# Kernel tuning notes

Hardware: AMD Instinct MI355X
Metric: run time of the kernel (lower is better)

The kernel has to match this reference:

```python
import jax, jax.numpy as jnp
import numpy as np

L = 3          # num_layers
D = 512        # hidden_dim
B, N = 8, 1024
EPS = 1e-5


def layernorm(x, gamma, beta):
    mu = jnp.mean(x, axis=-1, keepdims=True)
    var = jnp.var(x, axis=-1, keepdims=True)
    return (x - mu) * jax.lax.rsqrt(var + EPS) * gamma + beta


def setup_inputs() -> dict:
    key = jax.random.key(0)
    ks = jax.random.split(key, 12)
    s = 1.0 / np.sqrt(D)
    node_features = jax.random.normal(ks[0], (B, N, D), dtype=jnp.float32)
    adjacency_matrix = jax.random.randint(ks[1], (B, N, N), 0, 2, dtype=jnp.int32)
    return {
        "node_features": node_features,
        "adjacency_matrix": adjacency_matrix,
        # attn_linear: Linear(2D, 1) -> weight [2D], bias scalar, per layer
        "attn_w": jax.random.normal(ks[2], (L, 2 * D), dtype=jnp.float32) * (1.0 / np.sqrt(2 * D)),
        "attn_b": jax.random.normal(ks[3], (L,), dtype=jnp.float32) * 0.01,
        "W1": jax.random.normal(ks[4], (L, D, 4 * D), dtype=jnp.float32) * s,
        "b1": jnp.zeros((L, 4 * D), dtype=jnp.float32),
        "W2": jax.random.normal(ks[5], (L, 4 * D, D), dtype=jnp.float32) * (1.0 / np.sqrt(4 * D)),
        "b2": jnp.zeros((L, D), dtype=jnp.float32),
        "g1": jnp.ones((L, D), dtype=jnp.float32),
        "beta1": jnp.zeros((L, D), dtype=jnp.float32),
        "g2": jnp.ones((L, D), dtype=jnp.float32),
        "beta2": jnp.zeros((L, D), dtype=jnp.float32),
    }


def reference(node_features, adjacency_matrix, attn_w, attn_b, W1, b1, W2, b2, g1, beta1, g2, beta2):
    n = adjacency_matrix.shape[-1]
    # adjacency + self loops; mask of allowed edges
    mask = (adjacency_matrix.astype(jnp.float32) + jnp.eye(n, dtype=jnp.float32)) > 0  # [B,N,N]
    x = node_features
    d = x.shape[-1]
    for l in range(attn_w.shape[0]):
        # score_ij = a1.h_i + a2.h_j + b  (== Linear(concat(h_i,h_j)))
        si = x @ attn_w[l, :d]           # [B,N]
        sj = x @ attn_w[l, d:]           # [B,N]
        scores = si[:, :, None] + sj[:, None, :] + attn_b[l]   # [B,N,N]
        scores = jnp.where(scores >= 0, scores, 0.2 * scores)  # LeakyReLU(0.2)
        scores = jnp.where(mask, scores, -jnp.inf)
        attn = jax.nn.softmax(scores, axis=-1)                  # diag always unmasked
        agg = jnp.einsum('bij,bjd->bid', attn, x)
        h = layernorm(x + agg, g1[l], beta1[l])
        ff = jax.nn.gelu(h @ W1[l] + b1[l], approximate=False) @ W2[l] + b2[l]
        x = layernorm(h + ff, g2[l], beta2[l])
    return x
```

## Files before the change

### kernel.cpp

```cpp
#include <hip/hip_runtime.h>
#include <math.h>

#define NB 8
#define NN 1024
#define DD 512

typedef unsigned short u16;
typedef unsigned int u32;
typedef unsigned long long u64;
typedef __attribute__((ext_vector_type(8))) short bfrag;
typedef __attribute__((ext_vector_type(4))) float ffrag;

__device__ __forceinline__ u16 f2b(float f) {
    union { float f; u32 u; } v; v.f = f;
    u32 r = v.u + 0x7fffu + ((v.u >> 16) & 1u);
    return (u16)(r >> 16);
}
__device__ __forceinline__ float b2f(u16 b) {
    union { u32 u; float f; } v; v.u = ((u32)b) << 16;
    return v.f;
}

__device__ __forceinline__ float gelu_cheap(float v) {
    float s = v * 0.70710678118654752f;
    float a = fabsf(s);
    float t = 1.0f / (1.0f + 0.3275911f * a);
    float p = ((((1.061405429f * t - 1.453152027f) * t + 1.421413741f) * t
                - 0.284496736f) * t + 0.254829592f) * t;
    float erfa = 1.0f - p * __expf(-a * a);
    float erfs = copysignf(erfa, s);
    return 0.5f * v * (1.0f + erfs);
}

__device__ __forceinline__ void gload_lds16(const void* g, void* l) {
    __builtin_amdgcn_global_load_lds(
        (const __attribute__((address_space(1))) void*)g,
        (__attribute__((address_space(3))) void*)l, 16, 0, 0);
}

__global__ __launch_bounds__(256) void mask_pack(const int* __restrict__ adj,
                                                 u64* __restrict__ mb) {
    int idx = blockIdx.x * 256 + threadIdx.x;
    int w = idx & 15;
    int bi = idx >> 4;
    int i = bi & 1023;
    const int4* p = (const int4*)(adj + (size_t)bi * NN + w * 64);
    u64 m = 0;
#pragma unroll
    for (int q = 0; q < 16; ++q) {
        int4 v = p[q];
        if (v.x > 0) m |= 1ull << (q * 4 + 0);
        if (v.y > 0) m |= 1ull << (q * 4 + 1);
        if (v.z > 0) m |= 1ull << (q * 4 + 2);
        if (v.w > 0) m |= 1ull << (q * 4 + 3);
    }
    if (w == (i >> 6)) m |= 1ull << (i & 63);
    mb[idx] = m;
}

__global__ __launch_bounds__(256) void transpose_cvt(
    const float* __restrict__ in, u16* __restrict__ out,
    int R, int C, size_t inStr, size_t outStr)
{
    __shared__ float tile[32][33];
    int z = blockIdx.z;
    int r0 = blockIdx.y * 32, c0 = blockIdx.x * 32;
    int t = threadIdx.x;
    int tr = t >> 3, tc = (t & 7) * 4;
    float4 v = *(const float4*)(in + inStr * z + (size_t)(r0 + tr) * C + c0 + tc);
    tile[tr][tc + 0] = v.x; tile[tr][tc + 1] = v.y;
    tile[tr][tc + 2] = v.z; tile[tr][tc + 3] = v.w;
    __syncthreads();
    u32 w0 = (u32)f2b(tile[tc + 0][tr]) | ((u32)f2b(tile[tc + 1][tr]) << 16);
    u32 w1 = (u32)f2b(tile[tc + 2][tr]) | ((u32)f2b(tile[tc + 3][tr]) << 16);
    uint2 wv; wv.x = w0; wv.y = w1;
    *(uint2*)(out + outStr * z + (size_t)(c0 + tr) * R + r0 + tc) = wv;
}

__global__ __launch_bounds__(256) void score_proj_kernel(
    const float* __restrict__ x, const float* __restrict__ w,
    float* __restrict__ si, float* __restrict__ sj)
{
    int wave = threadIdx.x >> 6;
    int lane = threadIdx.x & 63;
    int row = blockIdx.x * 4 + wave;
    const float4* xr = (const float4*)(x + (size_t)row * DD) + lane * 2;
    const float4* w1 = (const float4*)(w) + lane * 2;
    const float4* w2 = (const float4*)(w + DD) + lane * 2;
    float a = 0.f, b2 = 0.f;
#pragma unroll
    for (int c = 0; c < 2; ++c) {
        float4 xv = xr[c], wa = w1[c], wb = w2[c];
        a  += xv.x * wa.x + xv.y * wa.y + xv.z * wa.z + xv.w * wa.w;
        b2 += xv.x * wb.x + xv.y * wb.y + xv.z * wb.z + xv.w * wb.w;
    }
#pragma unroll
    for (int off = 32; off > 0; off >>= 1) {
        a  += __shfl_xor(a, off);
        b2 += __shfl_xor(b2, off);
    }
    if (lane == 0) { si[row] = a; sj[row] = b2; }
}

__global__ __launch_bounds__(256) void softmax_p(
    const float* __restrict__ si, const float* __restrict__ sj,
    const float* __restrict__ attn_b, const u64* __restrict__ mb,
    u16* __restrict__ P)
{
    __shared__ u16 sb[8 * NN];
    int b  = blockIdx.x >> 7;
    int i0 = (blockIdx.x & 127) * 8;
    int tid = threadIdx.x;
    int r = tid >> 5, l32 = tid & 31;
    int i = i0 + r;
    float bb = attn_b[0];
    float siv = si[b * NN + i];
    const float* sjb = sj + b * NN;
    const u64* mbr = mb + ((size_t)b * NN + i) * 16;

    float sv[32];
    float mx = -INFINITY;
#pragma unroll
    for (int q = 0; q < 32; ++q) {
        int j = q * 32 + l32;
        u64 w = mbr[q >> 1];
        int bit = ((q & 1) << 5) + l32;
        float s = siv + sjb[j] + bb;
        s = (s >= 0.f) ? s : 0.2f * s;
        s = ((w >> bit) & 1ull) ? s : -INFINITY;
        sv[q] = s;
        mx = fmaxf(mx, s);
    }
#pragma unroll
    for (int off = 16; off > 0; off >>= 1) mx = fmaxf(mx, __shfl_xor(mx, off, 32));
    float sum = 0.f;
#pragma unroll
    for (int q = 0; q < 32; ++q) {
        float p = __expf(sv[q] - mx);
        sv[q] = p;
        sum += p;
    }
#pragma unroll
    for (int off = 16; off > 0; off >>= 1) sum += __shfl_xor(sum, off, 32);
    float inv = 1.f / sum;
#pragma unroll
    for (int q = 0; q < 32; ++q)
        sb[r * NN + q * 32 + l32] = f2b(sv[q] * inv);
    __syncthreads();
    const uint4* src = (const uint4*)sb;
    uint4* dst = (uint4*)(P + ((size_t)b * NN + i0) * NN);
#pragma unroll
    for (int t = 0; t < 4; ++t) dst[t * 256 + tid] = src[t * 256 + tid];
}

template <int EPI>
__global__ __launch_bounds__(256) void gemm64(
    const u16* __restrict__ A, const u16* __restrict__ Bm,
    const float* __restrict__ bias, const void* __restrict__ res,
    void* __restrict__ Cout, int K, int N, int lda, int ldb,
    size_t aStr, size_t bStr, size_t cStr, size_t resStr)
{
    __shared__ __align__(16) u16 lds[24576];
    int z = blockIdx.z;
    int m0 = blockIdx.y * 64, n0 = blockIdx.x * 128;
    int tid = threadIdx.x;
    int lane = tid & 63, wv = tid >> 6;

    const u16* ag[2]; const u16* bg[4];
    u32 la[2], lb[4];
#pragma unroll
    for (int i = 0; i < 2; ++i) {
        int q = i * 256 + tid;
        int row = q >> 3, c = q & 7;
        ag[i] = A + aStr * z + (size_t)(m0 + row) * lda + (c ^ (row & 7)) * 8;
        la[i] = i * 2048 + wv * 512;
    }
#pragma unroll
    for (int i = 0; i < 4; ++i) {
        int q = i * 256 + tid;
        int row = q >> 3, c = q & 7;
        bg[i] = Bm + bStr * z + (size_t)(n0 + row) * ldb + (c ^ (row & 7)) * 8;
        lb[i] = 8192 + i * 2048 + wv * 512;
    }

    int mw = (wv >> 1) * 32, nw = (wv & 1) * 64;
    int lr = lane & 15, lq = lane >> 4;
    int sw = lr & 7;

    ffrag acc[2][4];
#pragma unroll
    for (int i = 0; i < 2; ++i)
#pragma unroll
        for (int j = 0; j < 4; ++j) acc[i][j] = (ffrag){0.f, 0.f, 0.f, 0.f};

#pragma unroll
    for (int i = 0; i < 2; ++i) gload_lds16(ag[i], &lds[la[i]]);
#pragma unroll
    for (int i = 0; i < 4; ++i) gload_lds16(bg[i], &lds[lb[i]]);

    for (int k0 = 0; k0 < K; k0 += 64) {
        int cur = (k0 >> 6) & 1;
        if (k0 + 64 < K) {
#pragma unroll
            for (int i = 0; i < 2; ++i)
                gload_lds16(ag[i] + k0 + 64, &lds[((cur ^ 1) << 12) + la[i]]);
#pragma unroll
            for (int i = 0; i < 4; ++i)
                gload_lds16(bg[i] + k0 + 64, &lds[((cur ^ 1) << 13) + lb[i]]);
            asm volatile("s_waitcnt vmcnt(6)" ::: "memory");
        } else {
            asm volatile("s_waitcnt vmcnt(0)" ::: "memory");
        }
        asm volatile("s_barrier" ::: "memory");

        const u16* Ab = &lds[cur << 12];
        const u16* Bb = &lds[8192 + (cur << 13)];
#pragma unroll
        for (int h = 0; h < 2; ++h) {
            bfrag af[2], bf[4];
#pragma unroll
            for (int i = 0; i < 2; ++i)
                af[i] = *(const bfrag*)&Ab[(mw + i * 16 + lr) * 64 + ((h * 4 + lq) ^ sw) * 8];
#pragma unroll
            for (int j = 0; j < 4; ++j)
                bf[j] = *(const bfrag*)&Bb[(nw + j * 16 + lr) * 64 + ((h * 4 + lq) ^ sw) * 8];
#pragma unroll
            for (int i = 0; i < 2; ++i)
#pragma unroll
                for (int j = 0; j < 4; ++j)
                    acc[i][j] = __builtin_amdgcn_mfma_f32_16x16x32_bf16(af[i], bf[j], acc[i][j], 0, 0, 0);
        }
        asm volatile("s_waitcnt lgkmcnt(0)\ns_barrier" ::: "memory");
    }

    float* Cf = (float*)Cout + cStr * z;
    u16*   Cb = (u16*)Cout + cStr * z;
    const float* resf = (const float*)res;
    const u16*   resb = (const u16*)res;
#pragma unroll
    for (int i = 0; i < 2; ++i) {
        int row = m0 + mw + i * 16 + lq * 4;
#pragma unroll
        for (int j = 0; j < 4; ++j) {
            int col = n0 + nw + j * 16 + lr;
            float bv = (EPI != 0) ? bias[col] : 0.f;
#pragma unroll
            for (int r = 0; r < 4; ++r) {
                float v = acc[i][j][r] + bv;
                size_t off = (size_t)(row + r) * N + col;
                if (EPI == 1) {
                    Cb[off] = f2b(gelu_cheap(v));
                } else if (EPI == 0) {
                    Cf[off] = v + resf[resStr * z + off];
                } else {
                    Cf[off] = v + b2f(resb[off]);
                }
            }
        }
    }
}

template <bool BF>
__global__ __launch_bounds__(256) void ln_kernel(
    const float* __restrict__ in, const float* __restrict__ g,
    const float* __restrict__ be, void* __restrict__ out)
{
    int row = blockIdx.x;
    int tid = threadIdx.x;
    const float2* rp = (const float2*)(in + (size_t)row * DD);
    float2 v = rp[tid];
    float s  = v.x + v.y;
    float ss = v.x * v.x + v.y * v.y;
#pragma unroll
    for (int off = 32; off > 0; off >>= 1) {
        s  += __shfl_xor(s, off);
        ss += __shfl_xor(ss, off);
    }
    __shared__ float sh[8];
    int wave = tid >> 6, lane = tid & 63;
    if (lane == 0) { sh[wave] = s; sh[4 + wave] = ss; }
    __syncthreads();
    float S  = sh[0] + sh[1] + sh[2] + sh[3];
    float SS = sh[4] + sh[5] + sh[6] + sh[7];
    float mean = S * (1.f / DD);
    float var  = SS * (1.f / DD) - mean * mean;
    var = fmaxf(var, 0.f);
    float rs = rsqrtf(var + 1e-5f);
    float2 gv = ((const float2*)g)[tid];
    float2 bv = ((const float2*)be)[tid];
    float ox = (v.x - mean) * rs * gv.x + bv.x;
    float oy = (v.y - mean) * rs * gv.y + bv.y;
    if (BF) {
        u32 w = (u32)f2b(ox) | ((u32)f2b(oy) << 16);
        ((u32*)out)[(size_t)row * (DD / 2) + tid] = w;
    } else {
        float2 o; o.x = ox; o.y = oy;
        ((float2*)out)[(size_t)row * (DD / 2) + tid] = o;
    }
}

extern "C" void kernel_launch(void* const* d_in, const int* in_sizes, int n_in,
                              void* d_out, int out_size, void* d_ws, size_t ws_size,
                              hipStream_t stream) {
    const float* nf     = (const float*)d_in[0];
    const int*   adj    = (const int*)d_in[1];
    const float* attn_w = (const float*)d_in[2];
    const float* attn_b = (const float*)d_in[3];
    const float* W1     = (const float*)d_in[4];
    const float* b1     = (const float*)d_in[5];
    const float* W2     = (const float*)d_in[6];
    const float* b2     = (const float*)d_in[7];
    const float* g1     = (const float*)d_in[8];
    const float* be1    = (const float*)d_in[9];
    const float* g2     = (const float*)d_in[10];
    const float* be2    = (const float*)d_in[11];
    float* out = (float*)d_out;

    char* wsb = (char*)d_ws;
    float* x_cur = (float*)(wsb);
    u16*   h_bf  = (u16*)(wsb + 16777216);
    char*  scr   = wsb + 25165824;
    u16*   P     = (u16*)scr;
    float* hres  = (float*)(scr + 16777216);
    u16*   mid   = (u16*)scr;
    u16*   xT    = (u16*)(wsb + 58720256);
    u16*   W1t   = (u16*)(wsb + 67108864);
    u16*   W2t   = (u16*)(wsb + 73400320);
    u64*   mask  = (u64*)(wsb + 79691776);
    float* si    = (float*)(wsb + 80740352);
    float* sj    = (float*)(wsb + 80773120);

    mask_pack<<<512, 256, 0, stream>>>(adj, mask);
    transpose_cvt<<<dim3(64, 16, 3), 256, 0, stream>>>(W1, W1t, 512, 2048,
                                                       (size_t)512 * 2048, (size_t)512 * 2048);
    transpose_cvt<<<dim3(16, 64, 3), 256, 0, stream>>>(W2, W2t, 2048, 512,
                                                       (size_t)2048 * 512, (size_t)2048 * 512);

    for (int l = 0; l < 3; ++l) {
        const float* xin = (l == 0) ? nf : x_cur;
        score_proj_kernel<<<2048, 256, 0, stream>>>(xin, attn_w + (size_t)l * 1024, si, sj);
        transpose_cvt<<<dim3(16, 32, 8), 256, 0, stream>>>(xin, xT, 1024, 512,
                                                           (size_t)NN * DD, (size_t)NN * DD);
        softmax_p<<<1024, 256, 0, stream>>>(si, sj, attn_b + l, mask, P);
        gemm64<0><<<dim3(4, 16, 8), 256, 0, stream>>>(
            P, xT, nullptr, xin, hres, 1024, 512, 1024, 1024,
            (size_t)NN * NN, (size_t)DD * NN, (size_t)NN * DD, (size_t)NN * DD);
        ln_kernel<true><<<8192, 256, 0, stream>>>(hres, g1 + (size_t)l * 512, be1 + (size_t)l * 512, h_bf);
        gemm64<1><<<dim3(16, 128, 1), 256, 0, stream>>>(
            h_bf, W1t + (size_t)l * 1048576, b1 + (size_t)l * 2048, nullptr, mid,
            512, 2048, 512, 512, 0, 0, 0, 0);
        gemm64<2><<<dim3(4, 128, 1), 256, 0, stream>>>(
            mid, W2t + (size_t)l * 1048576, b2 + (size_t)l * 512, h_bf, x_cur,
            2048, 512, 2048, 2048, 0, 0, 0, 0);
        void* lnout = (l == 2) ? (void*)out : (void*)x_cur;
        ln_kernel<false><<<8192, 256, 0, stream>>>(x_cur, g2 + (size_t)l * 512, be2 + (size_t)l * 512, lnout);
    }
}
```

Measured before the change: 474.9 us.

## Triple-buffer GEMM loads, swizzle workgroups, stage GELU output, fuse score projection into LN

The GEMM moves from double to triple buffering in LDS, so two K tiles are in flight while the current one is computed. Workgroup IDs are remapped in strides of eight to spread neighbouring tiles across XCDs. The GELU epilogue now writes through LDS so global stores are coalesced 16-byte writes. The per-layer score projection kernel is folded into the preceding LayerNorm for layers 1 and 2, removing a launch and a re-read of x. The larger LDS footprint may reduce occupancy.

```diff
diff --git a/kernel.cpp b/kernel.cpp
--- a/kernel.cpp
+++ b/kernel.cpp
@@ -160,9 +160,15 @@
     void* __restrict__ Cout, int K, int N, int lda, int ldb,
     size_t aStr, size_t bStr, size_t cStr, size_t resStr)
 {
-    __shared__ __align__(16) u16 lds[24576];
-    int z = blockIdx.z;
-    int m0 = blockIdx.y * 64, n0 = blockIdx.x * 128;
+    __shared__ __align__(16) u16 lds[36864];
+    int gx = gridDim.x, gy = gridDim.y;
+    int wg = blockIdx.x + gx * (blockIdx.y + gy * blockIdx.z);
+    int nwg = gx * gy * gridDim.z;
+    wg = (wg & 7) * (nwg >> 3) + (wg >> 3);
+    int z = wg / (gx * gy);
+    int rem = wg - z * (gx * gy);
+    int by = rem / gx, bx = rem - by * gx;
+    int m0 = by * 64, n0 = bx * 128;
     int tid = threadIdx.x;
     int lane = tid & 63, wv = tid >> 6;
 
@@ -180,7 +186,7 @@
         int q = i * 256 + tid;
         int row = q >> 3, c = q & 7;
         bg[i] = Bm + bStr * z + (size_t)(n0 + row) * ldb + (c ^ (row & 7)) * 8;
-        lb[i] = 8192 + i * 2048 + wv * 512;
+        lb[i] = 4096 + i * 2048 + wv * 512;
     }
 
     int mw = (wv >> 1) * 32, nw = (wv & 1) * 64;
@@ -193,28 +199,35 @@
 #pragma unroll
         for (int j = 0; j < 4; ++j) acc[i][j] = (ffrag){0.f, 0.f, 0.f, 0.f};
 
+    int nt = K >> 6;
 #pragma unroll
     for (int i = 0; i < 2; ++i) gload_lds16(ag[i], &lds[la[i]]);
 #pragma unroll
     for (int i = 0; i < 4; ++i) gload_lds16(bg[i], &lds[lb[i]]);
-
-    for (int k0 = 0; k0 < K; k0 += 64) {
-        int cur = (k0 >> 6) & 1;
-        if (k0 + 64 < K) {
-#pragma unroll
-            for (int i = 0; i < 2; ++i)
-                gload_lds16(ag[i] + k0 + 64, &lds[((cur ^ 1) << 12) + la[i]]);
-#pragma unroll
-            for (int i = 0; i < 4; ++i)
-                gload_lds16(bg[i] + k0 + 64, &lds[((cur ^ 1) << 13) + lb[i]]);
+#pragma unroll
+    for (int i = 0; i < 2; ++i) gload_lds16(ag[i] + 64, &lds[12288 + la[i]]);
+#pragma unroll
+    for (int i = 0; i < 4; ++i) gload_lds16(bg[i] + 64, &lds[12288 + lb[i]]);
+
+    int cur = 0, stg = 2;
+    for (int t = 0; t < nt; ++t) {
+        if (t + 2 < nt) {
+            int bb = stg * 12288;
+            int ko = (t + 2) * 64;
+#pragma unroll
+            for (int i = 0; i < 2; ++i) gload_lds16(ag[i] + ko, &lds[bb + la[i]]);
+#pragma unroll
+            for (int i = 0; i < 4; ++i) gload_lds16(bg[i] + ko, &lds[bb + lb[i]]);
+            asm volatile("s_waitcnt vmcnt(12)" ::: "memory");
+        } else if (t + 2 == nt) {
             asm volatile("s_waitcnt vmcnt(6)" ::: "memory");
         } else {
             asm volatile("s_waitcnt vmcnt(0)" ::: "memory");
         }
         asm volatile("s_barrier" ::: "memory");
 
-        const u16* Ab = &lds[cur << 12];
-        const u16* Bb = &lds[8192 + (cur << 13)];
+        const u16* Ab = &lds[cur * 12288];
+        const u16* Bb = &lds[cur * 12288 + 4096];
 #pragma unroll
         for (int h = 0; h < 2; ++h) {
             bfrag af[2], bf[4];
@@ -231,39 +244,65 @@
                     acc[i][j] = __builtin_amdgcn_mfma_f32_16x16x32_bf16(af[i], bf[j], acc[i][j], 0, 0, 0);
         }
         asm volatile("s_waitcnt lgkmcnt(0)\ns_barrier" ::: "memory");
+        cur = (cur == 2) ? 0 : cur + 1;
+        stg = (stg == 2) ? 0 : stg + 1;
     }
 
     float* Cf = (float*)Cout + cStr * z;
     u16*   Cb = (u16*)Cout + cStr * z;
     const float* resf = (const float*)res;
     const u16*   resb = (const u16*)res;
-#pragma unroll
-    for (int i = 0; i < 2; ++i) {
-        int row = m0 + mw + i * 16 + lq * 4;
-#pragma unroll
-        for (int j = 0; j < 4; ++j) {
-            int col = n0 + nw + j * 16 + lr;
-            float bv = (EPI != 0) ? bias[col] : 0.f;
-#pragma unroll
-            for (int r = 0; r < 4; ++r) {
-                float v = acc[i][j][r] + bv;
-                size_t off = (size_t)(row + r) * N + col;
-                if (EPI == 1) {
-                    Cb[off] = f2b(gelu_cheap(v));
-                } else if (EPI == 0) {
-                    Cf[off] = v + resf[resStr * z + off];
-                } else {
-                    Cf[off] = v + b2f(resb[off]);
+    if (EPI == 1) {
+        u16* sb = lds;
+#pragma unroll
+        for (int i = 0; i < 2; ++i) {
+            int rr = mw + i * 16 + lq * 4;
+#pragma unroll
+            for (int j = 0; j < 4; ++j) {
+                int cc = nw + j * 16 + lr;
+                float bv = bias[n0 + cc];
+#pragma unroll
+                for (int r = 0; r < 4; ++r)
+                    sb[(rr + r) * 136 + cc] = f2b(gelu_cheap(acc[i][j][r] + bv));
+            }
+        }
+        __syncthreads();
+        u16* Crow = Cb + (size_t)m0 * N + n0;
+#pragma unroll
+        for (int t = 0; t < 4; ++t) {
+            int q = t * 256 + tid;
+            int row = q >> 4, c16 = q & 15;
+            *(uint4*)(Crow + (size_t)row * N + c16 * 8) =
+                *(const uint4*)(sb + row * 136 + c16 * 8);
+        }
+    } else {
+#pragma unroll
+        for (int i = 0; i < 2; ++i) {
+            int row = m0 + mw + i * 16 + lq * 4;
+#pragma unroll
+            for (int j = 0; j < 4; ++j) {
+                int col = n0 + nw + j * 16 + lr;
+                float bv = (EPI != 0) ? bias[col] : 0.f;
+#pragma unroll
+                for (int r = 0; r < 4; ++r) {
+                    float v = acc[i][j][r] + bv;
+                    size_t off = (size_t)(row + r) * N + col;
+                    if (EPI == 0) {
+                        Cf[off] = v + resf[resStr * z + off];
+                    } else {
+                        Cf[off] = v + b2f(resb[off]);
+                    }
                 }
             }
         }
     }
 }
 
-template <bool BF>
+template <bool BF, bool SP>
 __global__ __launch_bounds__(256) void ln_kernel(
     const float* __restrict__ in, const float* __restrict__ g,
-    const float* __restrict__ be, void* __restrict__ out)
+    const float* __restrict__ be, void* __restrict__ out,
+    const float* __restrict__ aw, float* __restrict__ si, float* __restrict__ sj)
 {
     int row = blockIdx.x;
     int tid = threadIdx.x;
@@ -297,6 +336,24 @@
         float2 o; o.x = ox; o.y = oy;
         ((float2*)out)[(size_t)row * (DD / 2) + tid] = o;
     }
+    if (SP) {
+        float2 wa = ((const float2*)aw)[tid];
+        float2 wb = ((const float2*)(aw + DD))[tid];
+        float a = ox * wa.x + oy * wa.y;
+        float c = ox * wb.x + oy * wb.y;
+#pragma unroll
+        for (int off = 32; off > 0; off >>= 1) {
+            a += __shfl_xor(a, off);
+            c += __shfl_xor(c, off);
+        }
+        __syncthreads();
+        if (lane == 0) { sh[wave] = a; sh[4 + wave] = c; }
+        __syncthreads();
+        if (tid == 0) {
+            si[row] = sh[0] + sh[1] + sh[2] + sh[3];
+            sj[row] = sh[4] + sh[5] + sh[6] + sh[7];
+        }
+    }
 }
 
 extern "C" void kernel_launch(void* const* d_in, const int* in_sizes, int n_in,
@@ -336,23 +393,32 @@
     transpose_cvt<<<dim3(16, 64, 3), 256, 0, stream>>>(W2, W2t, 2048, 512,
                                                        (size_t)2048 * 512, (size_t)2048 * 512);
 
+    score_proj_kernel<<<2048, 256, 0, stream>>>(nf, attn_w, si, sj);
+
     for (int l = 0; l < 3; ++l) {
         const float* xin = (l == 0) ? nf : x_cur;
-        score_proj_kernel<<<2048, 256, 0, stream>>>(xin, attn_w + (size_t)l * 1024, si, sj);
         transpose_cvt<<<dim3(16, 32, 8), 256, 0, stream>>>(xin, xT, 1024, 512,
                                                            (size_t)NN * DD, (size_t)NN * DD);
         softmax_p<<<1024, 256, 0, stream>>>(si, sj, attn_b + l, mask, P);
         gemm64<0><<<dim3(4, 16, 8), 256, 0, stream>>>(
             P, xT, nullptr, xin, hres, 1024, 512, 1024, 1024,
             (size_t)NN * NN, (size_t)DD * NN, (size_t)NN * DD, (size_t)NN * DD);
-        ln_kernel<true><<<8192, 256, 0, stream>>>(hres, g1 + (size_t)l * 512, be1 + (size_t)l * 512, h_bf);
+        ln_kernel<true, false><<<8192, 256, 0, stream>>>(
+            hres, g1 + (size_t)l * 512, be1 + (size_t)l * 512, h_bf, nullptr, nullptr, nullptr);
         gemm64<1><<<dim3(16, 128, 1), 256, 0, stream>>>(
             h_bf, W1t + (size_t)l * 1048576, b1 + (size_t)l * 2048, nullptr, mid,
             512, 2048, 512, 512, 0, 0, 0, 0);
         gemm64<2><<<dim3(4, 128, 1), 256, 0, stream>>>(
             mid, W2t + (size_t)l * 1048576, b2 + (size_t)l * 512, h_bf, x_cur,
             2048, 512, 2048, 2048, 0, 0, 0, 0);
-        void* lnout = (l == 2) ? (void*)out : (void*)x_cur;
-        ln_kernel<false><<<8192, 256, 0, stream>>>(x_cur, g2 + (size_t)l * 512, be2 + (size_t)l * 512, lnout);
-    }
-}
+        if (l < 2) {
+            ln_kernel<false, true><<<8192, 256, 0, stream>>>(
+                x_cur, g2 + (size_t)l * 512, be2 + (size_t)l * 512, x_cur,
+                attn_w + (size_t)(l + 1) * 1024, si, sj);
+        } else {
+            ln_kernel<false, false><<<8192, 256, 0, stream>>>(
+                x_cur, g2 + (size_t)l * 512, be2 + (size_t)l * 512, out,
+                nullptr, nullptr, nullptr);
+        }
+    }
+}
```

New measurement: 469.2 us. About the same (-1.2%).
